# Optimization experiments

Measured on AMD Instinct MI355X. Metric: run time of the kernel, lower is better.

## Reference

```python
import jax, jax.numpy as jnp
import numpy as np

B, S, D, H, V, N_SHARDS, CAP = 4, 512, 512, 8, 32000, 64, 128
HD = D // H


def _layernorm(x, g, b, eps=1e-5):
    mu = x.mean(-1, keepdims=True)
    var = ((x - mu) ** 2).mean(-1, keepdims=True)
    return (x - mu) * jax.lax.rsqrt(var + eps) * g + b


def setup_inputs() -> dict:
    key = jax.random.key(0)
    ks = jax.random.split(key, 16)
    s = 0.02
    return {
        'input_ids': jax.random.randint(ks[0], (B, S), 0, V, dtype=jnp.int32),
        'emb': jax.random.normal(ks[1], (V, D), jnp.float32) * s,
        'Wq': jax.random.normal(ks[2], (D, D), jnp.float32) * s,
        'Wk': jax.random.normal(ks[3], (D, D), jnp.float32) * s,
        'Wv': jax.random.normal(ks[4], (D, D), jnp.float32) * s,
        'Wo': jax.random.normal(ks[5], (D, D), jnp.float32) * s,
        'ln_g': jnp.ones((D,), jnp.float32),
        'ln_b': jnp.zeros((D,), jnp.float32),
        'W_router': jax.random.normal(ks[6], (D, N_SHARDS), jnp.float32),
        'mem_keys': jax.random.normal(ks[7], (N_SHARDS, CAP, D), jnp.float32) * s,
        'mem_values': jax.random.normal(ks[8], (N_SHARDS, CAP, D), jnp.float32) * s,
        'Wg_c': jax.random.normal(ks[9], (D, D), jnp.float32) * s,
        'Wg_m': jax.random.normal(ks[10], (D, D), jnp.float32) * s,
        'bg': jnp.zeros((D,), jnp.float32),
        'Wd': jax.random.normal(ks[11], (D, V), jnp.float32) * s,
        'bd': jnp.zeros((V,), jnp.float32),
        'top_k': 4,
    }


def reference(input_ids, emb, Wq, Wk, Wv, Wo, ln_g, ln_b, W_router,
              mem_keys, mem_values, Wg_c, Wg_m, bg, Wd, bd, top_k):
    # --- encode_context: embedding + causal MHA block (ContextSynthesizer) ---
    x = emb[input_ids]                                   # [B,S,D]
    q = (x @ Wq).reshape(B, S, H, HD)
    k = (x @ Wk).reshape(B, S, H, HD)
    v = (x @ Wv).reshape(B, S, H, HD)
    att = jnp.einsum('bqhd,bkhd->bhqk', q, k) / jnp.sqrt(jnp.float32(HD))
    causal = jnp.tril(jnp.ones((S, S), bool))
    att = jnp.where(causal[None, None], att, jnp.finfo(att.dtype).min)
    att = jax.nn.softmax(att, axis=-1)
    o = jnp.einsum('bhqk,bkhd->bqhd', att, v).reshape(B, S, D) @ Wo
    ctx = _layernorm(x + o, ln_g, ln_b)                  # [B,S,D]

    # --- LSHRouter: hyperplane projection -> shard id per token ---
    routes = jnp.argmax(ctx @ W_router, axis=-1)         # [B,S] int

    # --- MemoryShardStore.query, batched: per-token routed shard top-k read ---
    keys_g = mem_keys[routes]                            # [B,S,CAP,D] irregular gather
    scores = jnp.einsum('bscd,bsd->bsc', keys_g, ctx)    # [B,S,CAP]
    top_v, top_i = jax.lax.top_k(scores, top_k)          # [B,S,k]
    w = jax.nn.softmax(top_v, axis=-1)
    vals = mem_values[routes[:, :, None], top_i]         # [B,S,k,D]
    memory_stream = jnp.einsum('bsk,bskd->bsd', w, vals)

    # --- GatedMemoryFusion ---
    gate = jax.nn.sigmoid(ctx @ Wg_c + memory_stream @ Wg_m + bg)
    fused = gate * ctx + (1.0 - gate) * memory_stream

    # --- decoder; payload bias is zero (store holds no sequence_chunk records) ---
    logits = fused @ Wd + bd                             # [B,S,V]
    return logits
```

## Files before the change

### kernel.cpp

```cpp
#include <hip/hip_runtime.h>

typedef unsigned short u16;
typedef float f32x4 __attribute__((ext_vector_type(4)));
typedef short short8 __attribute__((ext_vector_type(8)));
typedef __bf16 bf16x8 __attribute__((ext_vector_type(8)));

#define B_  4
#define S_  512
#define D_  512
#define H_  8
#define HD_ 64
#define V_  32000
#define NSHARD_ 64
#define CAP_ 128
#define TOK_ (B_ * S_)

__device__ __forceinline__ float bf2f(u16 u) { return __uint_as_float(((unsigned)u) << 16); }
__device__ __forceinline__ u16 f2bf(float f) {
  unsigned u = __float_as_uint(f);
  u += 0x7FFFu + ((u >> 16) & 1u);
  return (u16)(u >> 16);
}

__device__ __forceinline__ f32x4 mfma16(short8 a, short8 b, f32x4 c) {
  return __builtin_amdgcn_mfma_f32_16x16x32_bf16(
      __builtin_bit_cast(bf16x8, a), __builtin_bit_cast(bf16x8, b), c, 0, 0, 0);
}

__device__ __forceinline__ void load_lds16(const void* g, void* l) {
  __builtin_amdgcn_global_load_lds(
      (const __attribute__((address_space(1))) void*)g,
      (__attribute__((address_space(3))) void*)l, 16, 0, 0);
}

template<int NS, bool ACC, int OM, bool CKLIM>
__global__ __launch_bounds__(256) void gemm_bt(
    const u16* __restrict__ Ah, const u16* __restrict__ Al, int ldA, long sA1, long sA2,
    const u16* __restrict__ Bh, const u16* __restrict__ Bl, int ldB, long sB1, long sB2,
    void* __restrict__ C0, void* __restrict__ C1, int ldC, long sC1, long sC2,
    int K, int z2n, float alpha)
{
  __shared__ u16 AsH[64 * 64];
  __shared__ u16 BsH[64 * 64];
  __shared__ u16 AsL[(NS == 3) ? 64 * 64 : 8];
  __shared__ u16 BsL[(NS == 3) ? 64 * 64 : 8];

  const int n0 = blockIdx.x * 64;
  const int m0 = blockIdx.y * 64;

  const int z = blockIdx.z;
  const int z1 = z / z2n, z2 = z - z1 * z2n;
  const long baseA = (long)z1 * sA1 + (long)z2 * sA2;
  const long baseB = (long)z1 * sB1 + (long)z2 * sB2;
  const long baseC = (long)z1 * sC1 + (long)z2 * sC2;

  const int tid = threadIdx.x;
  const int lane = tid & 63;
  const int w = tid >> 6;
  const int wm = (w >> 1) * 32, wn = (w & 1) * 32;
  const int fr = lane & 15, kg = lane >> 4;

  const int srow = lane >> 3;
  const int schunk = (lane & 7) ^ srow;

  const u16* gAh = Ah + baseA + (long)(m0 + w * 16 + srow) * ldA + schunk * 8;
  const u16* gBh = Bh + baseB + (long)(n0 + w * 16 + srow) * ldB + schunk * 8;
  const u16* gAl = (NS == 3) ? (Al + baseA + (long)(m0 + w * 16 + srow) * ldA + schunk * 8) : nullptr;
  const u16* gBl = (NS == 3) ? (Bl + baseB + (long)(n0 + w * 16 + srow) * ldB + schunk * 8) : nullptr;
  u16* lAh = &AsH[(w * 16) * 64];
  u16* lBh = &BsH[(w * 16) * 64];
  u16* lAl = &AsL[(NS == 3) ? (w * 16) * 64 : 0];
  u16* lBl = &BsL[(NS == 3) ? (w * 16) * 64 : 0];

  const int kmax = CKLIM ? (m0 + 64) : K;

  f32x4 acc[2][2] = {};

  for (int k0 = 0; k0 < kmax; k0 += 64) {
    load_lds16(gAh + k0, lAh);
    load_lds16(gAh + k0 + 8 * ldA, lAh + 8 * 64);
    load_lds16(gBh + k0, lBh);
    load_lds16(gBh + k0 + 8 * ldB, lBh + 8 * 64);
    if (NS == 3) {
      load_lds16(gAl + k0, lAl);
      load_lds16(gAl + k0 + 8 * ldA, lAl + 8 * 64);
      load_lds16(gBl + k0, lBl);
      load_lds16(gBl + k0 + 8 * ldB, lBl + 8 * 64);
    }
    __syncthreads();

    short8 ah[2][2], bh[2][2], al[2][2], bl[2][2];
#pragma unroll
    for (int mi = 0; mi < 2; ++mi) {
      int row = wm + mi * 16 + fr;
#pragma unroll
      for (int ks = 0; ks < 2; ++ks) {
        int idx = row * 64 + ((ks * 32 + kg * 8) ^ ((fr & 7) << 3));
        ah[mi][ks] = *(const short8*)&AsH[idx];
        if (NS == 3) al[mi][ks] = *(const short8*)&AsL[idx];
      }
    }
#pragma unroll
    for (int ni = 0; ni < 2; ++ni) {
      int row = wn + ni * 16 + fr;
#pragma unroll
      for (int ks = 0; ks < 2; ++ks) {
        int idx = row * 64 + ((ks * 32 + kg * 8) ^ ((fr & 7) << 3));
        bh[ni][ks] = *(const short8*)&BsH[idx];
        if (NS == 3) bl[ni][ks] = *(const short8*)&BsL[idx];
      }
    }
#pragma unroll
    for (int ks = 0; ks < 2; ++ks)
#pragma unroll
      for (int mi = 0; mi < 2; ++mi)
#pragma unroll
        for (int ni = 0; ni < 2; ++ni) {
          acc[mi][ni] = mfma16(ah[mi][ks], bh[ni][ks], acc[mi][ni]);
          if (NS == 3) {
            acc[mi][ni] = mfma16(ah[mi][ks], bl[ni][ks], acc[mi][ni]);
            acc[mi][ni] = mfma16(al[mi][ks], bh[ni][ks], acc[mi][ni]);
          }
        }
    __syncthreads();
  }

#pragma unroll
  for (int mi = 0; mi < 2; ++mi)
#pragma unroll
    for (int ni = 0; ni < 2; ++ni) {
      int gnc = n0 + wn + ni * 16 + fr;
#pragma unroll
      for (int r = 0; r < 4; ++r) {
        int gm = m0 + wm + mi * 16 + kg * 4 + r;
        float v = acc[mi][ni][r] * alpha;
        long idx = baseC + (long)gm * ldC + gnc;
        if (OM == 0) {
          float* C = (float*)C0;
          C[idx] = ACC ? (C[idx] + v) : v;
        } else {
          u16 h = f2bf(v);
          ((u16*)C0)[idx] = h;
          ((u16*)C1)[idx] = f2bf(v - bf2f(h));
        }
      }
    }
}

__global__ __launch_bounds__(256) void qkt_k(
    const u16* __restrict__ qkvh, const u16* __restrict__ qkvl,
    float* __restrict__ att)
{
  const int n0 = blockIdx.x * 64;
  const int m0 = blockIdx.y * 64;
  if (n0 > m0 + 63) return;
  const int z = blockIdx.z;
  const int b = z >> 3, h = z & 7;
  const long qbase = (long)b * 512 * 1536 + h * 64;
  const long kbase = qbase + 512;
  const long cbase = (long)z * 512 * 512;

  const int tid = threadIdx.x;
  const int lane = tid & 63;
  const int w = tid >> 6;
  const int wm = (w >> 1) * 32, wn = (w & 1) * 32;
  const int fr = lane & 15, kg = lane >> 4;

  short8 ah[2][2], al[2][2], bh[2][2], bl[2][2];
#pragma unroll
  for (int mi = 0; mi < 2; ++mi)
#pragma unroll
    for (int ks = 0; ks < 2; ++ks) {
      long ra = qbase + (long)(m0 + wm + mi * 16 + fr) * 1536 + ks * 32 + kg * 8;
      ah[mi][ks] = *(const short8*)(qkvh + ra);
      al[mi][ks] = *(const short8*)(qkvl + ra);
    }
#pragma unroll
  for (int ni = 0; ni < 2; ++ni)
#pragma unroll
    for (int ks = 0; ks < 2; ++ks) {
      long rb = kbase + (long)(n0 + wn + ni * 16 + fr) * 1536 + ks * 32 + kg * 8;
      bh[ni][ks] = *(const short8*)(qkvh + rb);
      bl[ni][ks] = *(const short8*)(qkvl + rb);
    }

  f32x4 acc[2][2] = {};
#pragma unroll
  for (int ks = 0; ks < 2; ++ks)
#pragma unroll
    for (int mi = 0; mi < 2; ++mi)
#pragma unroll
      for (int ni = 0; ni < 2; ++ni) {
        acc[mi][ni] = mfma16(ah[mi][ks], bh[ni][ks], acc[mi][ni]);
        acc[mi][ni] = mfma16(ah[mi][ks], bl[ni][ks], acc[mi][ni]);
        acc[mi][ni] = mfma16(al[mi][ks], bh[ni][ks], acc[mi][ni]);
      }

#pragma unroll
  for (int mi = 0; mi < 2; ++mi)
#pragma unroll
    for (int ni = 0; ni < 2; ++ni) {
      int gnc = n0 + wn + ni * 16 + fr;
#pragma unroll
      for (int r = 0; r < 4; ++r) {
        int gm = m0 + wm + mi * 16 + kg * 4 + r;
        att[cbase + (long)gm * 512 + gnc] = acc[mi][ni][r] * 0.125f;
      }
    }
}

__global__ __launch_bounds__(512, 4) void logits_gemm_bk32_k(
    const u16* __restrict__ A, const u16* __restrict__ Bt,
    const float* __restrict__ bias, float* __restrict__ C)
{
  __shared__ u16 As[2][256 * 32];
  __shared__ u16 Bs[2][128 * 32];

  const int id = blockIdx.x;
  const int swz = (id & 7) * 250 + (id >> 3);
  const int m0 = (swz & 7) * 256;
  const int n0 = (swz >> 3) * 128;

  const int tid = threadIdx.x;
  const int lane = tid & 63;
  const int wid = tid >> 6;
  const int wr = wid >> 1;
  const int wc = wid & 1;
  const int fr = lane & 15, kg = lane >> 4;
  const int srow = lane >> 2;
  const int schunk = (lane & 3) ^ (srow & 3);

  f32x4 acc[4][4] = {};
  short8 a[4], b[4];

  auto stage = [&](int kt) {
    const int buf = kt & 1;
    const long kc = (long)kt * 32 + schunk * 8;
    load_lds16(A + (long)(m0 + wid * 16 + srow) * D_ + kc,
               &As[buf][(wid * 16) * 32]);
    load_lds16(A + (long)(m0 + 128 + wid * 16 + srow) * D_ + kc,
               &As[buf][(128 + wid * 16) * 32]);
    load_lds16(Bt + (long)(n0 + wid * 16 + srow) * D_ + kc,
               &Bs[buf][(wid * 16) * 32]);
  };
  auto readfrags = [&](int buf) {
#pragma unroll
    for (int mi = 0; mi < 4; ++mi) {
      int row = wr * 64 + mi * 16 + fr;
      a[mi] = *(const short8*)&As[buf][row * 32 + ((kg ^ (row & 3)) * 8)];
    }
#pragma unroll
    for (int ni = 0; ni < 4; ++ni) {
      int row = wc * 64 + ni * 16 + fr;
      b[ni] = *(const short8*)&Bs[buf][row * 32 + ((kg ^ (row & 3)) * 8)];
    }
  };

  stage(0);
  stage(1);

  for (int t = 0; t < 16; ++t) {
    __builtin_amdgcn_sched_barrier(0);
    if (t < 15) { asm volatile("s_waitcnt vmcnt(3)" ::: "memory"); }
    else        { asm volatile("s_waitcnt vmcnt(0)" ::: "memory"); }
    __builtin_amdgcn_s_barrier();
    __builtin_amdgcn_sched_barrier(0);

    readfrags(t & 1);
    asm volatile("s_waitcnt lgkmcnt(0)" ::: "memory");
    __builtin_amdgcn_sched_barrier(0);
    __builtin_amdgcn_s_barrier();
    __builtin_amdgcn_sched_barrier(0);

    if (t + 2 < 16) stage(t + 2);

    __builtin_amdgcn_sched_barrier(0);
    __builtin_amdgcn_s_setprio(1);
#pragma unroll
    for (int mi = 0; mi < 4; ++mi)
#pragma unroll
      for (int ni = 0; ni < 4; ++ni)
        acc[mi][ni] = mfma16(a[mi], b[ni], acc[mi][ni]);
    __builtin_amdgcn_s_setprio(0);
    __builtin_amdgcn_sched_barrier(0);
  }

#pragma unroll
  for (int ni = 0; ni < 4; ++ni) {
    int gnc = n0 + wc * 64 + ni * 16 + fr;
    float bv = bias[gnc];
#pragma unroll
    for (int mi = 0; mi < 4; ++mi)
#pragma unroll
      for (int r = 0; r < 4; ++r) {
        int gm = m0 + wr * 64 + mi * 16 + kg * 4 + r;
        __builtin_nontemporal_store(acc[mi][ni][r] + bv, &C[(long)gm * V_ + gnc]);
      }
  }
}

template<bool LO>
__global__ __launch_bounds__(256) void transpose_split_k(
    const float* __restrict__ W, int ldw, int ldo, int koff,
    u16* __restrict__ oh, u16* __restrict__ ol)
{
  __shared__ float t[64][65];
  const int n0 = blockIdx.x * 64;
  const int k0 = blockIdx.y * 64;
  const int tid = threadIdx.x;
  {
    const int kk = tid >> 4;
    const int c4 = (tid & 15) * 4;
#pragma unroll
    for (int i = 0; i < 4; ++i) {
      f32x4 v = *(const f32x4*)(W + (long)(k0 + kk + i * 16) * ldw + n0 + c4);
      t[kk + i * 16][c4] = v[0];
      t[kk + i * 16][c4 + 1] = v[1];
      t[kk + i * 16][c4 + 2] = v[2];
      t[kk + i * 16][c4 + 3] = v[3];
    }
  }
  __syncthreads();
  {
    const int chunk = tid & 7;
    const int nn = tid >> 3;
#pragma unroll
    for (int j = 0; j < 2; ++j) {
      int n = nn + j * 32;
      u16 hbuf[8], lbuf[8];
#pragma unroll
      for (int e = 0; e < 8; ++e) {
        float fv = t[chunk * 8 + e][n];
        u16 h = f2bf(fv);
        hbuf[e] = h;
        if (LO) lbuf[e] = f2bf(fv - bf2f(h));
      }
      long ob = (long)(n0 + n) * ldo + koff + k0 + chunk * 8;
      *(short8*)(oh + ob) = *(short8*)hbuf;
      if (LO) *(short8*)(ol + ob) = *(short8*)lbuf;
    }
  }
}

__global__ __launch_bounds__(256) void v_transpose_k(
    const u16* __restrict__ qh, const u16* __restrict__ ql,
    u16* __restrict__ vTh, u16* __restrict__ vTl)
{
  __shared__ u16 th[64][68];
  __shared__ u16 tl[64][68];
  const int z = blockIdx.y;
  const int b = z >> 3, h = z & 7;
  const int s0 = blockIdx.x * 64;
  const long ibase = ((long)(b * 512 + s0)) * 1536 + 1024 + h * 64;
  const int tid = threadIdx.x;
  {
    const int sr = tid >> 2;
    const int c8 = (tid & 3) * 16;
    const long src = ibase + (long)sr * 1536 + c8;
    *(short8*)&th[sr][c8]     = *(const short8*)(qh + src);
    *(short8*)&th[sr][c8 + 8] = *(const short8*)(qh + src + 8);
    *(short8*)&tl[sr][c8]     = *(const short8*)(ql + src);
    *(short8*)&tl[sr][c8 + 8] = *(const short8*)(ql + src + 8);
  }
  __syncthreads();
  {
    const int dr = tid >> 2;
    const int s8 = (tid & 3) * 16;
    u16 oh[16], ol[16];
#pragma unroll
    for (int j = 0; j < 16; ++j) { oh[j] = th[s8 + j][dr]; ol[j] = tl[s8 + j][dr]; }
    long ob = (long)z * 64 * 512 + (long)dr * 512 + s0 + s8;
    *(short8*)(vTh + ob)     = *(short8*)&oh[0];
    *(short8*)(vTh + ob + 8) = *(short8*)&oh[8];
    *(short8*)(vTl + ob)     = *(short8*)&ol[0];
    *(short8*)(vTl + ob + 8) = *(short8*)&ol[8];
  }
}

__global__ __launch_bounds__(128) void embed_k(const int* __restrict__ ids,
                                               const float* __restrict__ emb,
                                               float* __restrict__ x,
                                               u16* __restrict__ xh,
                                               u16* __restrict__ xl) {
  const int t = blockIdx.x;
  const long id = ids[t];
  const int c = threadIdx.x * 4;
  f32x4 v = *(const f32x4*)(emb + id * (long)D_ + c);
  *(f32x4*)(x + (long)t * D_ + c) = v;
  u16 hh[4], ll[4];
#pragma unroll
  for (int j = 0; j < 4; ++j) {
    u16 h = f2bf(v[j]);
    hh[j] = h;
    ll[j] = f2bf(v[j] - bf2f(h));
  }
  *(unsigned long long*)(xh + (long)t * D_ + c) = *(unsigned long long*)hh;
  *(unsigned long long*)(xl + (long)t * D_ + c) = *(unsigned long long*)ll;
}

__global__ __launch_bounds__(64) void softmax_causal_k(
    const float* __restrict__ att, u16* __restrict__ ph, u16* __restrict__ pl) {
  const int row = blockIdx.x;
  const int i = row & 511;
  const long base = (long)row << 9;
  const float* p = att + base;
  const int lane = threadIdx.x;
  const int c0 = lane * 8;
  float v[8];
  float m = -3.4e38f;
  if (c0 <= i) {
    f32x4 a = *(const f32x4*)(p + c0);
    f32x4 b2 = *(const f32x4*)(p + c0 + 4);
#pragma unroll
    for (int j = 0; j < 8; ++j) {
      float x = (j < 4) ? a[j] : b2[j - 4];
      x = (c0 + j <= i) ? x : -3.4e38f;
      v[j] = x;
      m = fmaxf(m, x);
    }
  } else {
#pragma unroll
    for (int j = 0; j < 8; ++j) v[j] = 0.f;
  }
#pragma unroll
  for (int off = 32; off; off >>= 1) m = fmaxf(m, __shfl_xor(m, off));
  float s = 0.f;
  if (c0 <= i) {
#pragma unroll
    for (int j = 0; j < 8; ++j) {
      float e = (c0 + j <= i) ? expf(v[j] - m) : 0.f;
      v[j] = e;
      s += e;
    }
  }
#pragma unroll
  for (int off = 32; off; off >>= 1) s += __shfl_xor(s, off);
  float inv = 1.f / s;
  if (c0 <= (i | 63)) {
    u16 hh[8], ll[8];
#pragma unroll
    for (int j = 0; j < 8; ++j) {
      float e = (c0 <= i) ? v[j] * inv : 0.f;
      u16 h = f2bf(e);
      hh[j] = h;
      ll[j] = f2bf(e - bf2f(h));
    }
    *(short8*)(ph + base + c0) = *(short8*)hh;
    *(short8*)(pl + base + c0) = *(short8*)ll;
  }
}

__global__ __launch_bounds__(256) void resid_ln_k(
    const float* __restrict__ x, const float* __restrict__ proj,
    const float* __restrict__ g, const float* __restrict__ b,
    float* __restrict__ ctxf, u16* __restrict__ catA)
{
  const int t = blockIdx.x;
  const int tid = threadIdx.x;
  __shared__ float red[8];
  const float* xr = x + (long)t * D_;
  const float* pr = proj + (long)t * D_;
  float v0 = xr[tid] + pr[tid];
  float v1 = xr[tid + 256] + pr[tid + 256];
  float s = v0 + v1, q = v0 * v0 + v1 * v1;
#pragma unroll
  for (int off = 32; off; off >>= 1) { s += __shfl_xor(s, off); q += __shfl_xor(q, off); }
  const int wave = tid >> 6, lane = tid & 63;
  if (lane == 0) { red[wave] = s; red[4 + wave] = q; }
  __syncthreads();
  s = red[0] + red[1] + red[2] + red[3];
  q = red[4] + red[5] + red[6] + red[7];
  float mu = s * (1.f / 512.f);
  float var = q * (1.f / 512.f) - mu * mu;
  float rs = rsqrtf(var + 1e-5f);
  float o0 = (v0 - mu) * rs * g[tid] + b[tid];
  float o1 = (v1 - mu) * rs * g[tid + 256] + b[tid + 256];
  long base = (long)t * D_;
  ctxf[base + tid] = o0;
  ctxf[base + tid + 256] = o1;
  long cb = (long)t * 1024;
  catA[cb + tid] = f2bf(o0);
  catA[cb + tid + 256] = f2bf(o1);
}

__global__ __launch_bounds__(128) void route_mem_k(
    const float* __restrict__ ctxf, const float* __restrict__ Wr,
    const float* __restrict__ keys, const float* __restrict__ valsm,
    float* __restrict__ msf, u16* __restrict__ catA)
{
  const int t = blockIdx.x;
  const int tid = threadIdx.x;
  __shared__ float sctx[D_];
  __shared__ float spart[CAP_];
  __shared__ float sred2[2][64];
  __shared__ int s_route;
  __shared__ int sidx[4];
  __shared__ float sw[4];

  f32x4 cv = ((const f32x4*)(ctxf + (long)t * D_))[tid];
  ((f32x4*)sctx)[tid] = cv;
  __syncthreads();

  {
    const int c = tid & 63, half = tid >> 6;
    float accr = 0.f;
    const float* cp = sctx + half * 256;
    const float* wp = Wr + (long)(half * 256) * NSHARD_ + c;
    for (int d = 0; d < 256; ++d) accr += cp[d] * wp[(long)d * NSHARD_];
    sred2[half][c] = accr;
  }
  __syncthreads();
  if (tid < 64) {
    float v = sred2[0][tid] + sred2[1][tid];
    int idx = tid;
#pragma unroll
    for (int off = 32; off; off >>= 1) {
      float ov = __shfl_xor(v, off);
      int oi = __shfl_xor(idx, off);
      if (ov > v || (ov == v && oi < idx)) { v = ov; idx = oi; }
    }
    if (tid == 0) s_route = idx;
  }
  __syncthreads();
  const int route = s_route;

  {
    const float* krow = keys + ((long)route * CAP_ + tid) * D_;
    float sc = 0.f;
    for (int d0 = 0; d0 < D_; d0 += 4) {
      f32x4 kv = *(const f32x4*)(krow + d0);
      sc += sctx[d0] * kv[0] + sctx[d0 + 1] * kv[1] +
            sctx[d0 + 2] * kv[2] + sctx[d0 + 3] * kv[3];
    }
    spart[tid] = sc;
  }
  __syncthreads();

  for (int rep = 0; rep < 4; ++rep) {
    if (tid < 64) {
      float v1 = spart[tid]; int i1 = tid;
      float v2 = spart[tid + 64]; int i2 = tid + 64;
      float v; int idx;
      if (v2 > v1) { v = v2; idx = i2; } else { v = v1; idx = i1; }
#pragma unroll
      for (int off = 32; off; off >>= 1) {
        float ov = __shfl_xor(v, off);
        int oi = __shfl_xor(idx, off);
        if (ov > v || (ov == v && oi < idx)) { v = ov; idx = oi; }
      }
      if (tid == 0) { sidx[rep] = idx; sw[rep] = v; spart[idx] = -3.4e38f; }
    }
    __syncthreads();
  }

  float w0 = sw[0], w1 = sw[1], w2 = sw[2], w3 = sw[3];
  float mx = fmaxf(fmaxf(w0, w1), fmaxf(w2, w3));
  float e0 = expf(w0 - mx), e1 = expf(w1 - mx), e2 = expf(w2 - mx), e3 = expf(w3 - mx);
  float inv = 1.f / (e0 + e1 + e2 + e3);
  float wk[4] = {e0 * inv, e1 * inv, e2 * inv, e3 * inv};

  float a0 = 0, a1 = 0, a2 = 0, a3 = 0;
#pragma unroll
  for (int k = 0; k < 4; ++k) {
    const float* vr = valsm + ((long)route * CAP_ + sidx[k]) * D_ + tid * 4;
    f32x4 vv = *(const f32x4*)vr;
    float w = wk[k];
    a0 += w * vv[0]; a1 += w * vv[1]; a2 += w * vv[2]; a3 += w * vv[3];
  }
  f32x4 of; of[0] = a0; of[1] = a1; of[2] = a2; of[3] = a3;
  *(f32x4*)(msf + (long)t * D_ + tid * 4) = of;
  u16 oh[4];
  oh[0] = f2bf(a0); oh[1] = f2bf(a1); oh[2] = f2bf(a2); oh[3] = f2bf(a3);
  *(unsigned long long*)(catA + (long)t * 1024 + 512 + tid * 4) =
      *(unsigned long long*)oh;
}

__global__ __launch_bounds__(256) void gate_fuse_k(
    const float* __restrict__ g1, const float* __restrict__ bg,
    const float* __restrict__ ctxf, const float* __restrict__ msf,
    u16* __restrict__ fused)
{
  long base = ((long)blockIdx.x * 256 + threadIdx.x) * 4;
  f32x4 gv = *(const f32x4*)(g1 + base);
  f32x4 cv = *(const f32x4*)(ctxf + base);
  f32x4 mv = *(const f32x4*)(msf + base);
  int col = (int)(base & 511);
  u16 o[4];
#pragma unroll
  for (int j = 0; j < 4; ++j) {
    float g = 1.f / (1.f + expf(-(gv[j] + bg[col + j])));
    o[j] = f2bf(g * cv[j] + (1.f - g) * mv[j]);
  }
  *(unsigned long long*)(fused + base) = *(unsigned long long*)o;
}

extern "C" void kernel_launch(void* const* d_in, const int* in_sizes, int n_in,
                              void* d_out, int out_size, void* d_ws, size_t ws_size,
                              hipStream_t stream) {
  const int*   ids  = (const int*)d_in[0];
  const float* emb  = (const float*)d_in[1];
  const float* Wq   = (const float*)d_in[2];
  const float* Wk   = (const float*)d_in[3];
  const float* Wv   = (const float*)d_in[4];
  const float* Wo   = (const float*)d_in[5];
  const float* ln_g = (const float*)d_in[6];
  const float* ln_b = (const float*)d_in[7];
  const float* Wr   = (const float*)d_in[8];
  const float* mk   = (const float*)d_in[9];
  const float* mv   = (const float*)d_in[10];
  const float* Wgc  = (const float*)d_in[11];
  const float* Wgm  = (const float*)d_in[12];
  const float* bg   = (const float*)d_in[13];
  const float* Wd   = (const float*)d_in[14];
  const float* bd   = (const float*)d_in[15];
  float* out = (float*)d_out;

  char* ws = (char*)d_ws;
  size_t off = 0;
  auto alloc = [&](size_t bytes) -> void* {
    void* p = ws + off;
    off += (bytes + 255) & ~(size_t)255;
    return p;
  };
  float* x      = (float*)alloc((size_t)TOK_ * D_ * 4);
  u16*   xh     = (u16*)  alloc((size_t)TOK_ * D_ * 2);
  u16*   xl     = (u16*)  alloc((size_t)TOK_ * D_ * 2);
  u16*   wqkvTh = (u16*)  alloc((size_t)3 * D_ * D_ * 2);
  u16*   wqkvTl = (u16*)  alloc((size_t)3 * D_ * D_ * 2);
  u16*   woTh   = (u16*)  alloc((size_t)D_ * D_ * 2);
  u16*   woTl   = (u16*)  alloc((size_t)D_ * D_ * 2);
  u16*   wgT    = (u16*)  alloc((size_t)D_ * 1024 * 2);
  u16*   wdT    = (u16*)  alloc((size_t)D_ * V_ * 2);
  u16*   qkvh   = (u16*)  alloc((size_t)TOK_ * 3 * D_ * 2);
  u16*   qkvl   = (u16*)  alloc((size_t)TOK_ * 3 * D_ * 2);
  u16*   vTh    = (u16*)  alloc((size_t)B_ * H_ * HD_ * S_ * 2);
  u16*   vTl    = (u16*)  alloc((size_t)B_ * H_ * HD_ * S_ * 2);
  float* att    = (float*)alloc((size_t)B_ * H_ * S_ * S_ * 4);
  u16*   ph     = (u16*)  alloc((size_t)B_ * H_ * S_ * S_ * 2);
  u16*   pl     = (u16*)  alloc((size_t)B_ * H_ * S_ * S_ * 2);
  u16*   oh     = (u16*)  alloc((size_t)TOK_ * D_ * 2);
  u16*   ol     = (u16*)  alloc((size_t)TOK_ * D_ * 2);
  float* proj   = (float*)alloc((size_t)TOK_ * D_ * 4);
  float* ctxf   = (float*)alloc((size_t)TOK_ * D_ * 4);
  u16*   catA   = (u16*)  alloc((size_t)TOK_ * 1024 * 2);
  float* msf    = (float*)alloc((size_t)TOK_ * D_ * 4);
  float* g1     = (float*)alloc((size_t)TOK_ * D_ * 4);
  u16*   fused  = (u16*)  alloc((size_t)TOK_ * D_ * 2);

  {
    dim3 g8(D_ / 64, D_ / 64, 1);
    transpose_split_k<true><<<g8, 256, 0, stream>>>(Wq, D_, 512, 0, wqkvTh, wqkvTl);
    transpose_split_k<true><<<g8, 256, 0, stream>>>(Wk, D_, 512, 0, wqkvTh + D_ * D_, wqkvTl + D_ * D_);
    transpose_split_k<true><<<g8, 256, 0, stream>>>(Wv, D_, 512, 0, wqkvTh + 2 * D_ * D_, wqkvTl + 2 * D_ * D_);
    transpose_split_k<true><<<g8, 256, 0, stream>>>(Wo, D_, 512, 0, woTh, woTl);
    transpose_split_k<false><<<g8, 256, 0, stream>>>(Wgc, D_, 1024, 0, wgT, nullptr);
    transpose_split_k<false><<<g8, 256, 0, stream>>>(Wgm, D_, 1024, 512, wgT, nullptr);
    dim3 gd(V_ / 64, D_ / 64, 1);
    transpose_split_k<false><<<gd, 256, 0, stream>>>(Wd, V_, 512, 0, wdT, nullptr);
  }

  embed_k<<<TOK_, 128, 0, stream>>>(ids, emb, x, xh, xl);

  {
    dim3 g(1536 / 64, TOK_ / 64, 1);
    gemm_bt<3, false, 1, false><<<g, 256, 0, stream>>>(
        xh, xl, D_, 0, 0, wqkvTh, wqkvTl, D_, 0, 0,
        qkvh, qkvl, 1536, 0, 0, D_, 1, 1.f);
  }

  {
    dim3 g(S_ / 64, B_ * H_, 1);
    v_transpose_k<<<g, 256, 0, stream>>>(qkvh, qkvl, vTh, vTl);
  }

  {
    dim3 g(S_ / 64, S_ / 64, B_ * H_);
    qkt_k<<<g, 256, 0, stream>>>(qkvh, qkvl, att);
  }

  softmax_causal_k<<<B_ * H_ * S_, 64, 0, stream>>>(att, ph, pl);

  {
    dim3 g(1, S_ / 64, B_ * H_);
    gemm_bt<3, false, 1, true><<<g, 256, 0, stream>>>(
        ph, pl, S_, (long)H_ * S_ * S_, (long)S_ * S_,
        vTh, vTl, S_, (long)H_ * HD_ * S_, (long)HD_ * S_,
        oh, ol, D_, (long)S_ * D_, HD_,
        S_, H_, 1.f);
  }

  {
    dim3 g(D_ / 64, TOK_ / 64, 1);
    gemm_bt<3, false, 0, false><<<g, 256, 0, stream>>>(
        oh, ol, D_, 0, 0, woTh, woTl, D_, 0, 0,
        proj, nullptr, D_, 0, 0, D_, 1, 1.f);
  }

  resid_ln_k<<<TOK_, 256, 0, stream>>>(x, proj, ln_g, ln_b, ctxf, catA);

  route_mem_k<<<TOK_, 128, 0, stream>>>(ctxf, Wr, mk, mv, msf, catA);

  {
    dim3 g(D_ / 64, TOK_ / 64, 1);
    gemm_bt<1, false, 0, false><<<g, 256, 0, stream>>>(
        catA, nullptr, 1024, 0, 0, wgT, nullptr, 1024, 0, 0,
        g1, nullptr, D_, 0, 0, 1024, 1, 1.f);
  }

  gate_fuse_k<<<(TOK_ * D_) / (256 * 4), 256, 0, stream>>>(g1, bg, ctxf, msf, fused);

  logits_gemm_bk32_k<<<2000, 512, 0, stream>>>(fused, wdT, bd, out);
}
```

Baseline: 322.4 us.

## Fuse weight prep launches, layernorm with routing, and gate GEMM with fusion epilogue

Replaces the seven weight transpose/split launches with one kernel that dispatches on block index. Merges the residual layernorm into the routing/memory-read kernel, so ctx goes straight into shared memory instead of being reread from global. Replaces the generic gate GEMM plus its separate elementwise kernel with a dedicated GEMM whose epilogue applies bias, sigmoid and the gated blend, removing the g1 intermediate buffer. The cost is a more specialised gate GEMM and a runtime branch on the LO flag in weight prep.

```diff
diff --git a/kernel.cpp b/kernel.cpp
--- a/kernel.cpp
+++ b/kernel.cpp
@@ -147,6 +147,81 @@
     }
 }
 
+__global__ __launch_bounds__(256) void gate_gemm_k(
+    const u16* __restrict__ Ah, const u16* __restrict__ Bh,
+    const float* __restrict__ bgp, const float* __restrict__ ctxf,
+    const float* __restrict__ msf, u16* __restrict__ fused)
+{
+  __shared__ u16 AsH[64 * 64];
+  __shared__ u16 BsH[64 * 64];
+
+  const int n0 = blockIdx.x * 64;
+  const int m0 = blockIdx.y * 64;
+  const int tid = threadIdx.x;
+  const int lane = tid & 63;
+  const int w = tid >> 6;
+  const int wm = (w >> 1) * 32, wn = (w & 1) * 32;
+  const int fr = lane & 15, kg = lane >> 4;
+  const int srow = lane >> 3;
+  const int schunk = (lane & 7) ^ srow;
+
+  const u16* gAh = Ah + (long)(m0 + w * 16 + srow) * 1024 + schunk * 8;
+  const u16* gBh = Bh + (long)(n0 + w * 16 + srow) * 1024 + schunk * 8;
+  u16* lAh = &AsH[(w * 16) * 64];
+  u16* lBh = &BsH[(w * 16) * 64];
+
+  f32x4 acc[2][2] = {};
+
+  for (int k0 = 0; k0 < 1024; k0 += 64) {
+    load_lds16(gAh + k0, lAh);
+    load_lds16(gAh + k0 + 8 * 1024, lAh + 8 * 64);
+    load_lds16(gBh + k0, lBh);
+    load_lds16(gBh + k0 + 8 * 1024, lBh + 8 * 64);
+    __syncthreads();
+
+    short8 ah[2][2], bh[2][2];
+#pragma unroll
+    for (int mi = 0; mi < 2; ++mi) {
+      int row = wm + mi * 16 + fr;
+#pragma unroll
+      for (int ks = 0; ks < 2; ++ks)
+        ah[mi][ks] = *(const short8*)&AsH[row * 64 +
+                         ((ks * 32 + kg * 8) ^ ((fr & 7) << 3))];
+    }
+#pragma unroll
+    for (int ni = 0; ni < 2; ++ni) {
+      int row = wn + ni * 16 + fr;
+#pragma unroll
+      for (int ks = 0; ks < 2; ++ks)
+        bh[ni][ks] = *(const short8*)&BsH[row * 64 +
+                         ((ks * 32 + kg * 8) ^ ((fr & 7) << 3))];
+    }
+#pragma unroll
+    for (int ks = 0; ks < 2; ++ks)
+#pragma unroll
+      for (int mi = 0; mi < 2; ++mi)
+#pragma unroll
+        for (int ni = 0; ni < 2; ++ni)
+          acc[mi][ni] = mfma16(ah[mi][ks], bh[ni][ks], acc[mi][ni]);
+    __syncthreads();
+  }
+
+#pragma unroll
+  for (int mi = 0; mi < 2; ++mi)
+#pragma unroll
+    for (int ni = 0; ni < 2; ++ni) {
+      int gnc = n0 + wn + ni * 16 + fr;
+      float bv = bgp[gnc];
+#pragma unroll
+      for (int r = 0; r < 4; ++r) {
+        int gm = m0 + wm + mi * 16 + kg * 4 + r;
+        long idx = (long)gm * D_ + gnc;
+        float g = 1.f / (1.f + expf(-(acc[mi][ni][r] + bv)));
+        fused[idx] = f2bf(g * ctxf[idx] + (1.f - g) * msf[idx]);
+      }
+    }
+}
+
 __global__ __launch_bounds__(256) void qkt_k(
     const u16* __restrict__ qkvh, const u16* __restrict__ qkvl,
     float* __restrict__ att)
@@ -299,15 +374,39 @@
   }
 }
 
-template<bool LO>
-__global__ __launch_bounds__(256) void transpose_split_k(
-    const float* __restrict__ W, int ldw, int ldo, int koff,
-    u16* __restrict__ oh, u16* __restrict__ ol)
+__global__ __launch_bounds__(256) void prep_weights_k(
+    const float* __restrict__ Wq, const float* __restrict__ Wk,
+    const float* __restrict__ Wv, const float* __restrict__ Wo,
+    const float* __restrict__ Wgc, const float* __restrict__ Wgm,
+    const float* __restrict__ Wd,
+    u16* __restrict__ wqkvTh, u16* __restrict__ wqkvTl,
+    u16* __restrict__ woTh, u16* __restrict__ woTl,
+    u16* __restrict__ wgT, u16* __restrict__ wdT)
 {
+  const int bid = blockIdx.x;
+  const float* W; u16 *oh, *ol = nullptr;
+  int ldw, ldo, koff = 0, nb, kb;
+  bool LO = false;
+  if (bid < 384) {
+    const int w = bid >> 6, tt = bid & 63;
+    nb = tt & 7; kb = tt >> 3;
+    ldw = 512; ldo = 512;
+    switch (w) {
+      case 0: W = Wq;  oh = wqkvTh;               ol = wqkvTl;               LO = true; break;
+      case 1: W = Wk;  oh = wqkvTh + 512 * 512;   ol = wqkvTl + 512 * 512;   LO = true; break;
+      case 2: W = Wv;  oh = wqkvTh + 2 * 512 * 512; ol = wqkvTl + 2 * 512 * 512; LO = true; break;
+      case 3: W = Wo;  oh = woTh;                 ol = woTl;                 LO = true; break;
+      case 4: W = Wgc; oh = wgT; ldo = 1024; break;
+      default: W = Wgm; oh = wgT; ldo = 1024; koff = 512; break;
+    }
+  } else {
+    const int tt = bid - 384;
+    nb = tt % 500; kb = tt / 500;
+    W = Wd; ldw = V_; ldo = 512; oh = wdT;
+  }
+  const int n0 = nb * 64, k0 = kb * 64;
+  const int tid = threadIdx.x;
   __shared__ float t[64][65];
-  const int n0 = blockIdx.x * 64;
-  const int k0 = blockIdx.y * 64;
-  const int tid = threadIdx.x;
   {
     const int kk = tid >> 4;
     const int c4 = (tid & 15) * 4;
@@ -333,7 +432,7 @@
         float fv = t[chunk * 8 + e][n];
         u16 h = f2bf(fv);
         hbuf[e] = h;
-        if (LO) lbuf[e] = f2bf(fv - bf2f(h));
+        lbuf[e] = f2bf(fv - bf2f(h));
       }
       long ob = (long)(n0 + n) * ldo + koff + k0 + chunk * 8;
       *(short8*)(oh + ob) = *(short8*)hbuf;
@@ -450,64 +549,64 @@
   }
 }
 
-__global__ __launch_bounds__(256) void resid_ln_k(
+__global__ __launch_bounds__(128) void ln_route_k(
     const float* __restrict__ x, const float* __restrict__ proj,
     const float* __restrict__ g, const float* __restrict__ b,
-    float* __restrict__ ctxf, u16* __restrict__ catA)
-{
-  const int t = blockIdx.x;
-  const int tid = threadIdx.x;
-  __shared__ float red[8];
-  const float* xr = x + (long)t * D_;
-  const float* pr = proj + (long)t * D_;
-  float v0 = xr[tid] + pr[tid];
-  float v1 = xr[tid + 256] + pr[tid + 256];
-  float s = v0 + v1, q = v0 * v0 + v1 * v1;
-#pragma unroll
-  for (int off = 32; off; off >>= 1) { s += __shfl_xor(s, off); q += __shfl_xor(q, off); }
-  const int wave = tid >> 6, lane = tid & 63;
-  if (lane == 0) { red[wave] = s; red[4 + wave] = q; }
-  __syncthreads();
-  s = red[0] + red[1] + red[2] + red[3];
-  q = red[4] + red[5] + red[6] + red[7];
-  float mu = s * (1.f / 512.f);
-  float var = q * (1.f / 512.f) - mu * mu;
-  float rs = rsqrtf(var + 1e-5f);
-  float o0 = (v0 - mu) * rs * g[tid] + b[tid];
-  float o1 = (v1 - mu) * rs * g[tid + 256] + b[tid + 256];
-  long base = (long)t * D_;
-  ctxf[base + tid] = o0;
-  ctxf[base + tid + 256] = o1;
-  long cb = (long)t * 1024;
-  catA[cb + tid] = f2bf(o0);
-  catA[cb + tid + 256] = f2bf(o1);
-}
-
-__global__ __launch_bounds__(128) void route_mem_k(
-    const float* __restrict__ ctxf, const float* __restrict__ Wr,
-    const float* __restrict__ keys, const float* __restrict__ valsm,
-    float* __restrict__ msf, u16* __restrict__ catA)
+    const float* __restrict__ Wr, const float* __restrict__ keys,
+    const float* __restrict__ valsm,
+    float* __restrict__ ctxf, u16* __restrict__ catA, float* __restrict__ msf)
 {
   const int t = blockIdx.x;
   const int tid = threadIdx.x;
   __shared__ float sctx[D_];
+  __shared__ float red2[4];
   __shared__ float spart[CAP_];
   __shared__ float sred2[2][64];
   __shared__ int s_route;
   __shared__ int sidx[4];
   __shared__ float sw[4];
 
-  f32x4 cv = ((const f32x4*)(ctxf + (long)t * D_))[tid];
-  ((f32x4*)sctx)[tid] = cv;
+  const int c = tid * 4;
+  f32x4 xv = *(const f32x4*)(x + (long)t * D_ + c);
+  f32x4 pv = *(const f32x4*)(proj + (long)t * D_ + c);
+  float v0 = xv[0] + pv[0], v1 = xv[1] + pv[1];
+  float v2 = xv[2] + pv[2], v3 = xv[3] + pv[3];
+  float s = v0 + v1 + v2 + v3;
+  float q = v0 * v0 + v1 * v1 + v2 * v2 + v3 * v3;
+#pragma unroll
+  for (int off = 32; off; off >>= 1) { s += __shfl_xor(s, off); q += __shfl_xor(q, off); }
+  const int wave = tid >> 6, lane = tid & 63;
+  if (lane == 0) { red2[wave] = s; red2[2 + wave] = q; }
   __syncthreads();
-
-  {
-    const int c = tid & 63, half = tid >> 6;
+  s = red2[0] + red2[1];
+  q = red2[2] + red2[3];
+  float mu = s * (1.f / 512.f);
+  float var = q * (1.f / 512.f) - mu * mu;
+  float rs = rsqrtf(var + 1e-5f);
+  f32x4 gv = *(const f32x4*)(g + c);
+  f32x4 bv = *(const f32x4*)(b + c);
+  f32x4 of;
+  of[0] = (v0 - mu) * rs * gv[0] + bv[0];
+  of[1] = (v1 - mu) * rs * gv[1] + bv[1];
+  of[2] = (v2 - mu) * rs * gv[2] + bv[2];
+  of[3] = (v3 - mu) * rs * gv[3] + bv[3];
+  *(f32x4*)(ctxf + (long)t * D_ + c) = of;
+  ((f32x4*)sctx)[tid] = of;
+  {
+    u16 hh[4];
+#pragma unroll
+    for (int j = 0; j < 4; ++j) hh[j] = f2bf(of[j]);
+    *(unsigned long long*)(catA + (long)t * 1024 + c) = *(unsigned long long*)hh;
+  }
+  __syncthreads();
+
+  {
+    const int cc = tid & 63, half = tid >> 6;
     float accr = 0.f;
     const float* cp = sctx + half * 256;
-    const float* wp = Wr + (long)(half * 256) * NSHARD_ + c;
+    const float* wp = Wr + (long)(half * 256) * NSHARD_ + cc;
     for (int d = 0; d < 256; ++d) accr += cp[d] * wp[(long)d * NSHARD_];
-    sred2[half][c] = accr;
+    sred2[half][cc] = accr;
   }
   __syncthreads();
   if (tid < 64) {
@@ -538,10 +637,10 @@
 
   for (int rep = 0; rep < 4; ++rep) {
     if (tid < 64) {
-      float v1 = spart[tid]; int i1 = tid;
-      float v2 = spart[tid + 64]; int i2 = tid + 64;
+      float v1r = spart[tid]; int i1 = tid;
+      float v2r = spart[tid + 64]; int i2 = tid + 64;
       float v; int idx;
-      if (v2 > v1) { v = v2; idx = i2; } else { v = v1; idx = i1; }
+      if (v2r > v1r) { v = v2r; idx = i2; } else { v = v1r; idx = i1; }
 #pragma unroll
       for (int off = 32; off; off >>= 1) {
         float ov = __shfl_xor(v, off);
@@ -562,36 +661,17 @@
   float a0 = 0, a1 = 0, a2 = 0, a3 = 0;
 #pragma unroll
   for (int k = 0; k < 4; ++k) {
-    const float* vr = valsm + ((long)route * CAP_ + sidx[k]) * D_ + tid * 4;
+    const float* vr = valsm + ((long)route * CAP_ + sidx[k]) * D_ + c;
     f32x4 vv = *(const f32x4*)vr;
     float w = wk[k];
     a0 += w * vv[0]; a1 += w * vv[1]; a2 += w * vv[2]; a3 += w * vv[3];
   }
-  f32x4 of; of[0] = a0; of[1] = a1; of[2] = a2; of[3] = a3;
-  *(f32x4*)(msf + (long)t * D_ + tid * 4) = of;
+  f32x4 om; om[0] = a0; om[1] = a1; om[2] = a2; om[3] = a3;
+  *(f32x4*)(msf + (long)t * D_ + c) = om;
   u16 oh[4];
   oh[0] = f2bf(a0); oh[1] = f2bf(a1); oh[2] = f2bf(a2); oh[3] = f2bf(a3);
-  *(unsigned long long*)(catA + (long)t * 1024 + 512 + tid * 4) =
+  *(unsigned long long*)(catA + (long)t * 1024 + 512 + c) =
       *(unsigned long long*)oh;
-}
-
-__global__ __launch_bounds__(256) void gate_fuse_k(
-    const float* __restrict__ g1, const float* __restrict__ bg,
-    const float* __restrict__ ctxf, const float* __restrict__ msf,
-    u16* __restrict__ fused)
-{
-  long base = ((long)blockIdx.x * 256 + threadIdx.x) * 4;
-  f32x4 gv = *(const f32x4*)(g1 + base);
-  f32x4 cv = *(const f32x4*)(ctxf + base);
-  f32x4 mv = *(const f32x4*)(msf + base);
-  int col = (int)(base & 511);
-  u16 o[4];
-#pragma unroll
-  for (int j = 0; j < 4; ++j) {
-    float g = 1.f / (1.f + expf(-(gv[j] + bg[col + j])));
-    o[j] = f2bf(g * cv[j] + (1.f - g) * mv[j]);
-  }
-  *(unsigned long long*)(fused + base) = *(unsigned long long*)o;
 }
 
 extern "C" void kernel_launch(void* const* d_in, const int* in_sizes, int n_in,
@@ -644,20 +724,11 @@
   float* ctxf   = (float*)alloc((size_t)TOK_ * D_ * 4);
   u16*   catA   = (u16*)  alloc((size_t)TOK_ * 1024 * 2);
   float* msf    = (float*)alloc((size_t)TOK_ * D_ * 4);
-  float* g1     = (float*)alloc((size_t)TOK_ * D_ * 4);
   u16*   fused  = (u16*)  alloc((size_t)TOK_ * D_ * 2);
 
-  {
-    dim3 g8(D_ / 64, D_ / 64, 1);
-    transpose_split_k<true><<<g8, 256, 0, stream>>>(Wq, D_, 512, 0, wqkvTh, wqkvTl);
-    transpose_split_k<true><<<g8, 256, 0, stream>>>(Wk, D_, 512, 0, wqkvTh + D_ * D_, wqkvTl + D_ * D_);
-    transpose_split_k<true><<<g8, 256, 0, stream>>>(Wv, D_, 512, 0, wqkvTh + 2 * D_ * D_, wqkvTl + 2 * D_ * D_);
-    transpose_split_k<true><<<g8, 256, 0, stream>>>(Wo, D_, 512, 0, woTh, woTl);
-    transpose_split_k<false><<<g8, 256, 0, stream>>>(Wgc, D_, 1024, 0, wgT, nullptr);
-    transpose_split_k<false><<<g8, 256, 0, stream>>>(Wgm, D_, 1024, 512, wgT, nullptr);
-    dim3 gd(V_ / 64, D_ / 64, 1);
-    transpose_split_k<false><<<gd, 256, 0, stream>>>(Wd, V_, 512, 0, wdT, nullptr);
-  }
+  prep_weights_k<<<4384, 256, 0, stream>>>(
+      Wq, Wk, Wv, Wo, Wgc, Wgm, Wd,
+      wqkvTh, wqkvTl, woTh, woTl, wgT, wdT);
 
   embed_k<<<TOK_, 128, 0, stream>>>(ids, emb, x, xh, xl);
 
@@ -696,18 +767,13 @@
         proj, nullptr, D_, 0, 0, D_, 1, 1.f);
   }
 
-  resid_ln_k<<<TOK_, 256, 0, stream>>>(x, proj, ln_g, ln_b, ctxf, catA);
-
-  route_mem_k<<<TOK_, 128, 0, stream>>>(ctxf, Wr, mk, mv, msf, catA);
+  ln_route_k<<<TOK_, 128, 0, stream>>>(
+      x, proj, ln_g, ln_b, Wr, mk, mv, ctxf, catA, msf);
 
   {
     dim3 g(D_ / 64, TOK_ / 64, 1);
-    gemm_bt<1, false, 0, false><<<g, 256, 0, stream>>>(
-        catA, nullptr, 1024, 0, 0, wgT, nullptr, 1024, 0, 0,
-        g1, nullptr, D_, 0, 0, 1024, 1, 1.f);
-  }
-
-  gate_fuse_k<<<(TOK_ * D_) / (256 * 4), 256, 0, stream>>>(g1, bg, ctxf, msf, fused);
+    gate_gemm_k<<<g, 256, 0, stream>>>(catA, wgT, bg, ctxf, msf, fused);
+  }
 
   logits_gemm_bk32_k<<<2000, 512, 0, stream>>>(fused, wdT, bd, out);
 }
```

Measured after the change: 299.3 us. -7.2%, faster.
